# Kernel optimization log

Measured on AMD Instinct MI355X. Metric: run time of the kernel, lower is better.

## Reference

```python
import jax, jax.numpy as jnp
import numpy as np

N = 20000          # nodes
E = 320000         # edges
H = 128            # hidden_channels
A = 512            # aerial feature dim
SPOT = 20000
DIST_UNIT = 50
NEMB = SPOT // DIST_UNIT
RATIO = 0.25       # neighbor_ratio


def setup_inputs() -> dict:
    key = jax.random.key(0)
    ks = jax.random.split(key, 12)
    x = jax.random.normal(ks[0], (N, H), jnp.float32)
    edge_index = jax.random.randint(ks[1], (2, E), 0, N)
    distances = jax.random.randint(ks[2], (E,), 0, SPOT)
    aerial_emb = jax.random.normal(ks[3], (N, A), jnp.float32)
    s = lambda k, shape, fan: jax.random.normal(k, shape, jnp.float32) / np.sqrt(fan).astype(np.float32)
    W_lin = s(ks[4], (H, H), H)
    b_lin = jnp.zeros((H,), jnp.float32)
    W_q = s(ks[5], (H + A + H, H), H + A + H)
    b_q = jnp.zeros((H,), jnp.float32)
    W_v = s(ks[6], (H, H), H)
    b_v = jnp.zeros((H,), jnp.float32)
    dist_table = jax.random.normal(ks[7], (NEMB, H), jnp.float32)  # init.normal_ like torch
    W_l = s(ks[8], (H, H), H)   # SAGE lin_l (neighbor aggr), with bias
    b_l = jnp.zeros((H,), jnp.float32)
    W_r = s(ks[9], (H, H), H)   # SAGE lin_r (root), no bias in PyG default
    return dict(x=x, edge_index=edge_index, distances=distances, aerial_emb=aerial_emb,
                W_lin=W_lin, b_lin=b_lin, W_q=W_q, b_q=b_q, W_v=W_v, b_v=b_v,
                dist_table=dist_table, W_l=W_l, b_l=b_l, W_r=W_r)


def reference(x, edge_index, distances, aerial_emb, W_lin, b_lin, W_q, b_q, W_v, b_v, dist_table, W_l, b_l, W_r):
    n = x.shape[0]
    e = edge_index.shape[1]
    k = int(e * RATIO)  # static: number of sampled edges

    x = x @ W_lin + b_lin                                  # [N, H]
    src, tgt = edge_index[0], edge_index[1]
    source_x = x[src]                                      # [E, H]
    target_x = x[tgt]                                      # [E, H]
    source_aerial = aerial_emb[src]                        # [E, A]
    dist_x = dist_table[distances // DIST_UNIT]            # [E, H]

    query = jnp.concatenate([source_x, source_aerial, dist_x], axis=1) @ W_q + b_q  # [E, H]
    value = target_x @ W_v + b_v                           # [E, H]
    logits = -jnp.linalg.norm(query - value, axis=1)       # [E]
    logprob = jax.nn.log_softmax(logits, axis=0)

    # torch.multinomial(prob, k) without replacement == Gumbel top-k on log-probs
    u = jax.random.uniform(jax.random.key(42), (e,), jnp.float32)
    gumbel = -jnp.log(-jnp.log(u + 1e-20) + 1e-20)
    _, sel = jax.lax.top_k(logprob + gumbel, k)            # [k] selected edge ids
    src_s = src[sel]
    tgt_s = tgt[sel]

    # SAGEConv (mean aggregation): out = lin_l(mean_j x_j) + lin_r(x)
    msg = jax.ops.segment_sum(x[src_s], tgt_s, num_segments=n)              # [N, H]
    deg = jax.ops.segment_sum(jnp.ones((k,), x.dtype), tgt_s, num_segments=n)
    aggr = msg / jnp.maximum(deg, 1.0)[:, None]
    out = aggr @ W_l + b_l + x @ W_r                       # [N, H]
    return out
```

## Files before the change

kernel.cpp:

```cpp
#include <hip/hip_runtime.h>
#include <stdint.h>

#define N_NODES 20000
#define E_EDGES 320000
#define H_DIM 128
#define A_DIM 512
#define NEMB_N 400
#define K_SEL 80000u
#define NB1 16384
#define NB2 16384
#define CAND_MAX 8192
#define LO_F (-128.0f)
#define SCALE1 (16384.0f / 160.0f)

struct SelState {
    int b1; unsigned cum1; unsigned r1;
    int b2; unsigned cum2; unsigned r2;
    unsigned long long T;
};

__device__ __forceinline__ uint32_t rotl32(uint32_t x, int r) {
    return (x << r) | (x >> (32 - r));
}

__device__ __forceinline__ void threefry2x32(uint32_t k0, uint32_t k1,
                                             uint32_t& x0, uint32_t& x1) {
    uint32_t ks0 = k0, ks1 = k1, ks2 = k0 ^ k1 ^ 0x1BD11BDAu;
    x0 += ks0; x1 += ks1;
    x0 += x1; x1 = rotl32(x1, 13); x1 ^= x0;
    x0 += x1; x1 = rotl32(x1, 15); x1 ^= x0;
    x0 += x1; x1 = rotl32(x1, 26); x1 ^= x0;
    x0 += x1; x1 = rotl32(x1, 6);  x1 ^= x0;
    x0 += ks1; x1 += ks2 + 1u;
    x0 += x1; x1 = rotl32(x1, 17); x1 ^= x0;
    x0 += x1; x1 = rotl32(x1, 29); x1 ^= x0;
    x0 += x1; x1 = rotl32(x1, 16); x1 ^= x0;
    x0 += x1; x1 = rotl32(x1, 24); x1 ^= x0;
    x0 += ks2; x1 += ks0 + 2u;
    x0 += x1; x1 = rotl32(x1, 13); x1 ^= x0;
    x0 += x1; x1 = rotl32(x1, 15); x1 ^= x0;
    x0 += x1; x1 = rotl32(x1, 26); x1 ^= x0;
    x0 += x1; x1 = rotl32(x1, 6);  x1 ^= x0;
    x0 += ks0; x1 += ks1 + 3u;
    x0 += x1; x1 = rotl32(x1, 17); x1 ^= x0;
    x0 += x1; x1 = rotl32(x1, 29); x1 ^= x0;
    x0 += x1; x1 = rotl32(x1, 16); x1 ^= x0;
    x0 += x1; x1 = rotl32(x1, 24); x1 ^= x0;
    x0 += ks1; x1 += ks2 + 4u;
    x0 += x1; x1 = rotl32(x1, 13); x1 ^= x0;
    x0 += x1; x1 = rotl32(x1, 15); x1 ^= x0;
    x0 += x1; x1 = rotl32(x1, 26); x1 ^= x0;
    x0 += x1; x1 = rotl32(x1, 6);  x1 ^= x0;
    x0 += ks2; x1 += ks0 + 5u;
}

__global__ __launch_bounds__(256) void k_rand(float* __restrict__ u) {
    int e = blockIdx.x * 256 + threadIdx.x;
    if (e >= E_EDGES) return;
    uint32_t x0 = 0u, x1 = (uint32_t)e;
    threefry2x32(0u, 42u, x0, x1);
    uint32_t bits = x0 ^ x1;
    uint32_t fb = (bits >> 9) | 0x3f800000u;
    u[e] = __uint_as_float(fb) - 1.0f;
}

__global__ __launch_bounds__(128) void k_node(
    const float* __restrict__ x, const float* __restrict__ aerial,
    const float* __restrict__ Wlin, const float* __restrict__ blin,
    const float* __restrict__ Wq, const float* __restrict__ bq,
    const float* __restrict__ Wv, const float* __restrict__ bv,
    float* __restrict__ xl32, float* __restrict__ q32, float* __restrict__ v32) {
    __shared__ float xinT[H_DIM][8];
    __shared__ float xsT[H_DIM][8];
    __shared__ float aerT[A_DIM][8];
    const int j = threadIdx.x;
    const int n0 = blockIdx.x * 8;
#pragma unroll
    for (int m = 0; m < 8; ++m) xinT[j][m] = x[(size_t)(n0 + m) * H_DIM + j];
#pragma unroll
    for (int m = 0; m < 8; ++m)
#pragma unroll
        for (int c = 0; c < 4; ++c)
            aerT[c * H_DIM + j][m] = aerial[(size_t)(n0 + m) * A_DIM + c * H_DIM + j];
    __syncthreads();
    float acc[8];
    {
        float bj = blin[j];
#pragma unroll
        for (int m = 0; m < 8; ++m) acc[m] = bj;
        for (int k = 0; k < H_DIM; ++k) {
            float w = Wlin[k * H_DIM + j];
            const float4* xp = (const float4*)&xinT[k][0];
            float4 a0 = xp[0], a1 = xp[1];
            acc[0] = fmaf(a0.x, w, acc[0]); acc[1] = fmaf(a0.y, w, acc[1]);
            acc[2] = fmaf(a0.z, w, acc[2]); acc[3] = fmaf(a0.w, w, acc[3]);
            acc[4] = fmaf(a1.x, w, acc[4]); acc[5] = fmaf(a1.y, w, acc[5]);
            acc[6] = fmaf(a1.z, w, acc[6]); acc[7] = fmaf(a1.w, w, acc[7]);
        }
    }
#pragma unroll
    for (int m = 0; m < 8; ++m) {
        xsT[j][m] = acc[m];
        xl32[(size_t)(n0 + m) * H_DIM + j] = acc[m];
    }
    __syncthreads();
    {
        float bj = bv[j];
        float av[8];
#pragma unroll
        for (int m = 0; m < 8; ++m) av[m] = bj;
        for (int k = 0; k < H_DIM; ++k) {
            float w = Wv[k * H_DIM + j];
            const float4* xp = (const float4*)&xsT[k][0];
            float4 a0 = xp[0], a1 = xp[1];
            av[0] = fmaf(a0.x, w, av[0]); av[1] = fmaf(a0.y, w, av[1]);
            av[2] = fmaf(a0.z, w, av[2]); av[3] = fmaf(a0.w, w, av[3]);
            av[4] = fmaf(a1.x, w, av[4]); av[5] = fmaf(a1.y, w, av[5]);
            av[6] = fmaf(a1.z, w, av[6]); av[7] = fmaf(a1.w, w, av[7]);
        }
#pragma unroll
        for (int m = 0; m < 8; ++m) v32[(size_t)(n0 + m) * H_DIM + j] = av[m];
    }
    {
        float bj = bq[j];
        float aq[8];
#pragma unroll
        for (int m = 0; m < 8; ++m) aq[m] = bj;
        for (int k = 0; k < H_DIM; ++k) {
            float w = Wq[k * H_DIM + j];
            const float4* xp = (const float4*)&xsT[k][0];
            float4 a0 = xp[0], a1 = xp[1];
            aq[0] = fmaf(a0.x, w, aq[0]); aq[1] = fmaf(a0.y, w, aq[1]);
            aq[2] = fmaf(a0.z, w, aq[2]); aq[3] = fmaf(a0.w, w, aq[3]);
            aq[4] = fmaf(a1.x, w, aq[4]); aq[5] = fmaf(a1.y, w, aq[5]);
            aq[6] = fmaf(a1.z, w, aq[6]); aq[7] = fmaf(a1.w, w, aq[7]);
        }
        for (int k = 0; k < A_DIM; ++k) {
            float w = Wq[(size_t)(H_DIM + k) * H_DIM + j];
            const float4* xp = (const float4*)&aerT[k][0];
            float4 a0 = xp[0], a1 = xp[1];
            aq[0] = fmaf(a0.x, w, aq[0]); aq[1] = fmaf(a0.y, w, aq[1]);
            aq[2] = fmaf(a0.z, w, aq[2]); aq[3] = fmaf(a0.w, w, aq[3]);
            aq[4] = fmaf(a1.x, w, aq[4]); aq[5] = fmaf(a1.y, w, aq[5]);
            aq[6] = fmaf(a1.z, w, aq[6]); aq[7] = fmaf(a1.w, w, aq[7]);
        }
#pragma unroll
        for (int m = 0; m < 8; ++m) q32[(size_t)(n0 + m) * H_DIM + j] = aq[m];
    }
}

__global__ __launch_bounds__(128) void k_dist(
    const float* __restrict__ dtab, const float* __restrict__ Wq,
    float* __restrict__ dq32) {
    __shared__ float dsT[H_DIM][8];
    const int j = threadIdx.x;
    const int n0 = blockIdx.x * 8;
#pragma unroll
    for (int m = 0; m < 8; ++m) dsT[j][m] = dtab[(size_t)(n0 + m) * H_DIM + j];
    __syncthreads();
    float acc[8];
#pragma unroll
    for (int m = 0; m < 8; ++m) acc[m] = 0.0f;
    for (int k = 0; k < H_DIM; ++k) {
        float w = Wq[(size_t)(H_DIM + A_DIM + k) * H_DIM + j];
        const float4* xp = (const float4*)&dsT[k][0];
        float4 a0 = xp[0], a1 = xp[1];
        acc[0] = fmaf(a0.x, w, acc[0]); acc[1] = fmaf(a0.y, w, acc[1]);
        acc[2] = fmaf(a0.z, w, acc[2]); acc[3] = fmaf(a0.w, w, acc[3]);
        acc[4] = fmaf(a1.x, w, acc[4]); acc[5] = fmaf(a1.y, w, acc[5]);
        acc[6] = fmaf(a1.z, w, acc[6]); acc[7] = fmaf(a1.w, w, acc[7]);
    }
#pragma unroll
    for (int m = 0; m < 8; ++m) dq32[(size_t)(n0 + m) * H_DIM + j] = acc[m];
}

__device__ __forceinline__ int bin1_of(float s) {
    float t = (s - LO_F) * SCALE1;
    int b = (int)t;
    return min(max(b, 0), NB1 - 1);
}
__device__ __forceinline__ int bin2_of(float s, int b1) {
    float t = (s - LO_F) * SCALE1;
    float frac = t - (float)b1;
    int b = (int)(frac * (float)NB2);
    return min(max(b, 0), NB2 - 1);
}

__global__ __launch_bounds__(256) void k_score(
    const int* __restrict__ ei, const int* __restrict__ dist,
    const float* __restrict__ q32, const float* __restrict__ v32,
    const float* __restrict__ dq32, const float* __restrict__ u,
    unsigned long long* __restrict__ keys, float* __restrict__ s32o,
    unsigned* __restrict__ hist1) {
    const int half = threadIdx.x >> 5, lane = threadIdx.x & 31;
    const int e = blockIdx.x * 8 + half;
    const int s = ei[e], t = ei[E_EDGES + e];
    const int db = dist[e] / 50;
    const float4* qp = (const float4*)(q32 + (size_t)s * H_DIM);
    const float4* vp = (const float4*)(v32 + (size_t)t * H_DIM);
    const float4* dp = (const float4*)(dq32 + (size_t)db * H_DIM);
    float4 q = qp[lane], v = vp[lane], d = dp[lane];
    float dx = q.x + d.x - v.x;
    float dy = q.y + d.y - v.y;
    float dz = q.z + d.z - v.z;
    float dw = q.w + d.w - v.w;
    float ss = fmaf(dx, dx, fmaf(dy, dy, fmaf(dz, dz, dw * dw)));
#pragma unroll
    for (int o = 16; o > 0; o >>= 1) ss += __shfl_xor(ss, o, 64);
    if (lane == 0) {
        float nrm = sqrtf(ss);
        float uu = u[e];
        float a = -logf(uu + 1e-20f);
        float g = -logf(a + 1e-20f);
        float score = g - nrm;
        int ib = __float_as_int(score);
        unsigned m32 = (ib < 0) ? ~(unsigned)ib : ((unsigned)ib | 0x80000000u);
        keys[e] = ((unsigned long long)m32 << 32) | (unsigned)(0xFFFFFFFFu - (unsigned)e);
        s32o[e] = score;
        atomicAdd(&hist1[bin1_of(score)], 1u);
    }
}

__global__ __launch_bounds__(256) void k_hist2(const float* __restrict__ s32,
                                               const SelState* __restrict__ st,
                                               unsigned* __restrict__ hist2) {
    int e = blockIdx.x * 256 + threadIdx.x;
    if (e >= E_EDGES) return;
    float s = s32[e];
    int b1 = bin1_of(s);
    if (b1 != st->b1) return;
    atomicAdd(&hist2[bin2_of(s, b1)], 1u);
}

__global__ __launch_bounds__(256) void k_scan(const unsigned* __restrict__ hist,
                                              SelState* st, int phase) {
    __shared__ unsigned csum[256];
    __shared__ unsigned bins[64];
    __shared__ int selc;
    __shared__ unsigned cumbase;
    const int t = threadIdx.x;
    const unsigned target = (phase == 1) ? K_SEL : st->r1;
    unsigned s = 0;
    for (int i = 0; i < 64; ++i) s += hist[t * 64 + i];
    csum[t] = s;
    __syncthreads();
    if (t == 0) {
        unsigned cum = 0; int c = 255;
        for (; c >= 0; --c) {
            if (cum + csum[c] >= target) break;
            cum += csum[c];
        }
        selc = c; cumbase = cum;
    }
    __syncthreads();
    if (t < 64) bins[t] = hist[selc * 64 + t];
    __syncthreads();
    if (t == 0) {
        unsigned cum = cumbase; int b = -1;
        for (int i = 63; i >= 0; --i) {
            if (cum + bins[i] >= target) { b = selc * 64 + i; break; }
            cum += bins[i];
        }
        unsigned r = target - cum;
        if (phase == 1) { st->b1 = b; st->cum1 = cum; st->r1 = r; }
        else           { st->b2 = b; st->cum2 = cum; st->r2 = r; }
    }
}

__global__ __launch_bounds__(256) void k_collect(
    const float* __restrict__ s32, const unsigned long long* __restrict__ keys,
    const SelState* __restrict__ st, unsigned long long* __restrict__ cand,
    unsigned* __restrict__ cnt) {
    int e = blockIdx.x * 256 + threadIdx.x;
    if (e >= E_EDGES) return;
    float s = s32[e];
    int b1 = bin1_of(s);
    if (b1 != st->b1) return;
    if (bin2_of(s, b1) != st->b2) return;
    unsigned p = atomicAdd(cnt, 1u);
    if (p < CAND_MAX) cand[p] = keys[e];
}

__global__ __launch_bounds__(256) void k_thresh(
    const unsigned long long* __restrict__ cand, const unsigned* __restrict__ cnt,
    SelState* st) {
    int c = (int)min(*cnt, (unsigned)CAND_MAX);
    unsigned r2 = st->r2;
    for (int i = threadIdx.x; i < c; i += blockDim.x) {
        unsigned long long ki = cand[i];
        unsigned g = 0;
        for (int j = 0; j < c; ++j) g += (cand[j] > ki);
        if (g == r2 - 1) st->T = ki;
    }
}

__global__ __launch_bounds__(256) void k_scatter(
    const int* __restrict__ ei, const unsigned long long* __restrict__ keys,
    const SelState* __restrict__ st, const float* __restrict__ xl32,
    float* __restrict__ msg, float* __restrict__ deg) {
    const int wid = threadIdx.x >> 6, lane = threadIdx.x & 63;
    const int e = blockIdx.x * 4 + wid;
    if (keys[e] >= st->T) {
        int sidx = ei[e], tidx = ei[E_EDGES + e];
        const float* xp = xl32 + (size_t)sidx * H_DIM;
        float* mp = msg + (size_t)tidx * H_DIM;
        const int h = lane * 2;
        atomicAdd(&mp[h], xp[h]);
        atomicAdd(&mp[h + 1], xp[h + 1]);
        if (lane == 0) atomicAdd(&deg[tidx], 1.0f);
    }
}

__global__ __launch_bounds__(128) void k_out(
    const float* __restrict__ msg, const float* __restrict__ deg,
    const float* __restrict__ xl32, const float* __restrict__ Wl,
    const float* __restrict__ bl, const float* __restrict__ Wr,
    float* __restrict__ out) {
    __shared__ float axT[H_DIM][8];
    __shared__ float xxT[H_DIM][8];
    const int j = threadIdx.x;
    const int n0 = blockIdx.x * 8;
#pragma unroll
    for (int m = 0; m < 8; ++m) {
        float d = fmaxf(deg[n0 + m], 1.0f);
        axT[j][m] = msg[(size_t)(n0 + m) * H_DIM + j] / d;
        xxT[j][m] = xl32[(size_t)(n0 + m) * H_DIM + j];
    }
    __syncthreads();
    float acc[8];
    float bj = bl[j];
#pragma unroll
    for (int m = 0; m < 8; ++m) acc[m] = bj;
    for (int k = 0; k < H_DIM; ++k) {
        float wl = Wl[k * H_DIM + j];
        float wr = Wr[k * H_DIM + j];
        const float4* ap = (const float4*)&axT[k][0];
        const float4* xp = (const float4*)&xxT[k][0];
        float4 a0 = ap[0], a1 = ap[1];
        float4 x0 = xp[0], x1 = xp[1];
        acc[0] = fmaf(a0.x, wl, fmaf(x0.x, wr, acc[0]));
        acc[1] = fmaf(a0.y, wl, fmaf(x0.y, wr, acc[1]));
        acc[2] = fmaf(a0.z, wl, fmaf(x0.z, wr, acc[2]));
        acc[3] = fmaf(a0.w, wl, fmaf(x0.w, wr, acc[3]));
        acc[4] = fmaf(a1.x, wl, fmaf(x1.x, wr, acc[4]));
        acc[5] = fmaf(a1.y, wl, fmaf(x1.y, wr, acc[5]));
        acc[6] = fmaf(a1.z, wl, fmaf(x1.z, wr, acc[6]));
        acc[7] = fmaf(a1.w, wl, fmaf(x1.w, wr, acc[7]));
    }
#pragma unroll
    for (int m = 0; m < 8; ++m) out[(size_t)(n0 + m) * H_DIM + j] = acc[m];
}

extern "C" void kernel_launch(void* const* d_in, const int* in_sizes, int n_in,
                              void* d_out, int out_size, void* d_ws, size_t ws_size,
                              hipStream_t stream) {
    const float* x      = (const float*)d_in[0];
    const int*   ei     = (const int*)d_in[1];
    const int*   dist   = (const int*)d_in[2];
    const float* aerial = (const float*)d_in[3];
    const float* Wlin   = (const float*)d_in[4];
    const float* blin   = (const float*)d_in[5];
    const float* Wq     = (const float*)d_in[6];
    const float* bq     = (const float*)d_in[7];
    const float* Wv     = (const float*)d_in[8];
    const float* bv     = (const float*)d_in[9];
    const float* dtab   = (const float*)d_in[10];
    const float* Wl     = (const float*)d_in[11];
    const float* bl     = (const float*)d_in[12];
    const float* Wr     = (const float*)d_in[13];
    float* out = (float*)d_out;

    char* ws = (char*)d_ws;
    size_t off = 0;
    auto alloc = [&](size_t bytes) -> void* {
        void* p = ws + off;
        off += (bytes + 255) & ~(size_t)255;
        return p;
    };
    float* q32  = (float*)alloc((size_t)N_NODES * H_DIM * 4);
    float* v32  = (float*)alloc((size_t)N_NODES * H_DIM * 4);
    float* dq32 = (float*)alloc((size_t)NEMB_N * H_DIM * 4);
    unsigned long long* keys = (unsigned long long*)alloc((size_t)E_EDGES * 8);
    float* xl32 = (float*)alloc((size_t)N_NODES * H_DIM * 4);
    float* urnd = (float*)alloc((size_t)E_EDGES * 4);
    float* s32  = (float*)alloc((size_t)E_EDGES * 4);
    char* zbase = ws + off;
    float* msg  = (float*)alloc((size_t)N_NODES * H_DIM * 4);
    float* deg  = (float*)alloc((size_t)N_NODES * 4);
    unsigned* hist1 = (unsigned*)alloc((size_t)NB1 * 4);
    unsigned* hist2 = (unsigned*)alloc((size_t)NB2 * 4);
    unsigned long long* cand = (unsigned long long*)alloc((size_t)CAND_MAX * 8);
    unsigned* counters = (unsigned*)alloc(256);
    SelState* st = (SelState*)alloc(256);
    size_t zlen = (size_t)((ws + off) - zbase);

    hipMemsetAsync(zbase, 0, zlen, stream);

    k_node<<<N_NODES / 8, 128, 0, stream>>>(x, aerial, Wlin, blin, Wq, bq, Wv, bv,
                                            xl32, q32, v32);
    k_dist<<<NEMB_N / 8, 128, 0, stream>>>(dtab, Wq, dq32);
    k_rand<<<(E_EDGES + 255) / 256, 256, 0, stream>>>(urnd);
    k_score<<<E_EDGES / 8, 256, 0, stream>>>(ei, dist, q32, v32, dq32, urnd, keys, s32, hist1);
    k_scan<<<1, 256, 0, stream>>>(hist1, st, 1);
    k_hist2<<<(E_EDGES + 255) / 256, 256, 0, stream>>>(s32, st, hist2);
    k_scan<<<1, 256, 0, stream>>>(hist2, st, 2);
    k_collect<<<(E_EDGES + 255) / 256, 256, 0, stream>>>(s32, keys, st, cand, &counters[0]);
    k_thresh<<<1, 256, 0, stream>>>(cand, &counters[0], st);
    k_scatter<<<E_EDGES / 4, 256, 0, stream>>>(ei, keys, st, xl32, msg, deg);
    k_out<<<N_NODES / 8, 128, 0, stream>>>(msg, deg, xl32, Wl, bl, Wr, out);
}
```

Measured before the change: 553.9 us.

## Counting-sort edges by source node and swizzle block order for gather locality

Adds a counting sort of the edges by source node (histogram, single-block prefix scan, atomic placement), so the score and scatter kernels walk edges grouped by source and reuse the q32/xl32 rows they gather. Block indices in those kernels are swizzled across the 8 groups, presumably to spread work over the XCDs. Keys and scores are stored in sorted order while keeping the original edge id in the key, so selection results and tie-breaking stay the same. The cost is three extra kernel launches, extra atomics and about 16 bytes per edge of extra index traffic, which are meant to be repaid by better cache hits on the gathers.

```diff
diff --git a/kernel.cpp b/kernel.cpp
--- a/kernel.cpp
+++ b/kernel.cpp
@@ -174,6 +174,51 @@
     for (int m = 0; m < 8; ++m) dq32[(size_t)(n0 + m) * H_DIM + j] = acc[m];
 }
 
+__global__ __launch_bounds__(256) void k_hist_src(const int* __restrict__ ei,
+                                                  unsigned* __restrict__ cnt) {
+    int e = blockIdx.x * 256 + threadIdx.x;
+    if (e >= E_EDGES) return;
+    atomicAdd(&cnt[ei[e]], 1u);
+}
+
+__global__ __launch_bounds__(256) void k_prefix(const unsigned* __restrict__ cnt,
+                                                unsigned* __restrict__ off) {
+    __shared__ unsigned ssum[256];
+    const int t = threadIdx.x;
+    const int PER = (N_NODES + 255) / 256;
+    unsigned s = 0;
+    for (int i = 0; i < PER; ++i) {
+        int idx = t * PER + i;
+        if (idx < N_NODES) s += cnt[idx];
+    }
+    ssum[t] = s;
+    __syncthreads();
+    if (t == 0) {
+        unsigned acc = 0;
+        for (int i = 0; i < 256; ++i) { unsigned v = ssum[i]; ssum[i] = acc; acc += v; }
+    }
+    __syncthreads();
+    unsigned run = ssum[t];
+    for (int i = 0; i < PER; ++i) {
+        int idx = t * PER + i;
+        if (idx < N_NODES) { off[idx] = run; run += cnt[idx]; }
+    }
+}
+
+__global__ __launch_bounds__(256) void k_place(
+    const int* __restrict__ ei, const int* __restrict__ dist,
+    unsigned* __restrict__ off_work, int* __restrict__ srcsort,
+    int* __restrict__ tgtsort, int* __restrict__ dbsort, int* __restrict__ esort) {
+    int e = blockIdx.x * 256 + threadIdx.x;
+    if (e >= E_EDGES) return;
+    int s = ei[e];
+    unsigned pos = atomicAdd(&off_work[s], 1u);
+    srcsort[pos] = s;
+    tgtsort[pos] = ei[E_EDGES + e];
+    dbsort[pos] = dist[e] / 50;
+    esort[pos] = e;
+}
+
 __device__ __forceinline__ int bin1_of(float s) {
     float t = (s - LO_F) * SCALE1;
     int b = (int)t;
@@ -187,15 +232,19 @@
 }
 
 __global__ __launch_bounds__(256) void k_score(
-    const int* __restrict__ ei, const int* __restrict__ dist,
+    const int* __restrict__ srcsort, const int* __restrict__ tgtsort,
+    const int* __restrict__ dbsort, const int* __restrict__ esort,
     const float* __restrict__ q32, const float* __restrict__ v32,
     const float* __restrict__ dq32, const float* __restrict__ u,
-    unsigned long long* __restrict__ keys, float* __restrict__ s32o,
+    unsigned long long* __restrict__ keys_s, float* __restrict__ s32o,
     unsigned* __restrict__ hist1) {
     const int half = threadIdx.x >> 5, lane = threadIdx.x & 31;
-    const int e = blockIdx.x * 8 + half;
-    const int s = ei[e], t = ei[E_EDGES + e];
-    const int db = dist[e] / 50;
+    const int nb = E_EDGES / 8;
+    const int bid = blockIdx.x;
+    const int swz = (bid & 7) * (nb >> 3) + (bid >> 3);
+    const int i = swz * 8 + half;
+    const int s = srcsort[i], t = tgtsort[i];
+    const int db = dbsort[i];
     const float4* qp = (const float4*)(q32 + (size_t)s * H_DIM);
     const float4* vp = (const float4*)(v32 + (size_t)t * H_DIM);
     const float4* dp = (const float4*)(dq32 + (size_t)db * H_DIM);
@@ -208,6 +257,7 @@
 #pragma unroll
     for (int o = 16; o > 0; o >>= 1) ss += __shfl_xor(ss, o, 64);
     if (lane == 0) {
+        const int e = esort[i];
         float nrm = sqrtf(ss);
         float uu = u[e];
         float a = -logf(uu + 1e-20f);
@@ -215,8 +265,8 @@
         float score = g - nrm;
         int ib = __float_as_int(score);
         unsigned m32 = (ib < 0) ? ~(unsigned)ib : ((unsigned)ib | 0x80000000u);
-        keys[e] = ((unsigned long long)m32 << 32) | (unsigned)(0xFFFFFFFFu - (unsigned)e);
-        s32o[e] = score;
+        keys_s[i] = ((unsigned long long)m32 << 32) | (unsigned)(0xFFFFFFFFu - (unsigned)e);
+        s32o[i] = score;
         atomicAdd(&hist1[bin1_of(score)], 1u);
     }
 }
@@ -295,13 +345,17 @@
 }
 
 __global__ __launch_bounds__(256) void k_scatter(
-    const int* __restrict__ ei, const unsigned long long* __restrict__ keys,
+    const int* __restrict__ srcsort, const int* __restrict__ tgtsort,
+    const unsigned long long* __restrict__ keys_s,
     const SelState* __restrict__ st, const float* __restrict__ xl32,
     float* __restrict__ msg, float* __restrict__ deg) {
     const int wid = threadIdx.x >> 6, lane = threadIdx.x & 63;
-    const int e = blockIdx.x * 4 + wid;
-    if (keys[e] >= st->T) {
-        int sidx = ei[e], tidx = ei[E_EDGES + e];
+    const int nb = E_EDGES / 4;
+    const int bid = blockIdx.x;
+    const int swz = (bid & 7) * (nb >> 3) + (bid >> 3);
+    const int i = swz * 4 + wid;
+    if (keys_s[i] >= st->T) {
+        int sidx = srcsort[i], tidx = tgtsort[i];
         const float* xp = xl32 + (size_t)sidx * H_DIM;
         float* mp = msg + (size_t)tidx * H_DIM;
         const int h = lane * 2;
@@ -380,15 +434,21 @@
     float* q32  = (float*)alloc((size_t)N_NODES * H_DIM * 4);
     float* v32  = (float*)alloc((size_t)N_NODES * H_DIM * 4);
     float* dq32 = (float*)alloc((size_t)NEMB_N * H_DIM * 4);
-    unsigned long long* keys = (unsigned long long*)alloc((size_t)E_EDGES * 8);
     float* xl32 = (float*)alloc((size_t)N_NODES * H_DIM * 4);
     float* urnd = (float*)alloc((size_t)E_EDGES * 4);
-    float* s32  = (float*)alloc((size_t)E_EDGES * 4);
+    int* srcsort = (int*)alloc((size_t)E_EDGES * 4);
+    int* tgtsort = (int*)alloc((size_t)E_EDGES * 4);
+    int* dbsort  = (int*)alloc((size_t)E_EDGES * 4);
+    int* esort   = (int*)alloc((size_t)E_EDGES * 4);
+    unsigned long long* keys_s = (unsigned long long*)alloc((size_t)E_EDGES * 8);
+    float* s32_s = (float*)alloc((size_t)E_EDGES * 4);
+    unsigned* off_work = (unsigned*)alloc((size_t)N_NODES * 4);
     char* zbase = ws + off;
     float* msg  = (float*)alloc((size_t)N_NODES * H_DIM * 4);
     float* deg  = (float*)alloc((size_t)N_NODES * 4);
     unsigned* hist1 = (unsigned*)alloc((size_t)NB1 * 4);
     unsigned* hist2 = (unsigned*)alloc((size_t)NB2 * 4);
+    unsigned* cnt_src = (unsigned*)alloc((size_t)N_NODES * 4);
     unsigned long long* cand = (unsigned long long*)alloc((size_t)CAND_MAX * 8);
     unsigned* counters = (unsigned*)alloc(256);
     SelState* st = (SelState*)alloc(256);
@@ -396,16 +456,23 @@
 
     hipMemsetAsync(zbase, 0, zlen, stream);
 
+    k_hist_src<<<(E_EDGES + 255) / 256, 256, 0, stream>>>(ei, cnt_src);
+    k_prefix<<<1, 256, 0, stream>>>(cnt_src, off_work);
+    k_place<<<(E_EDGES + 255) / 256, 256, 0, stream>>>(ei, dist, off_work,
+                                                       srcsort, tgtsort, dbsort, esort);
+
     k_node<<<N_NODES / 8, 128, 0, stream>>>(x, aerial, Wlin, blin, Wq, bq, Wv, bv,
                                             xl32, q32, v32);
     k_dist<<<NEMB_N / 8, 128, 0, stream>>>(dtab, Wq, dq32);
     k_rand<<<(E_EDGES + 255) / 256, 256, 0, stream>>>(urnd);
-    k_score<<<E_EDGES / 8, 256, 0, stream>>>(ei, dist, q32, v32, dq32, urnd, keys, s32, hist1);
+
+    k_score<<<E_EDGES / 8, 256, 0, stream>>>(srcsort, tgtsort, dbsort, esort,
+                                             q32, v32, dq32, urnd, keys_s, s32_s, hist1);
     k_scan<<<1, 256, 0, stream>>>(hist1, st, 1);
-    k_hist2<<<(E_EDGES + 255) / 256, 256, 0, stream>>>(s32, st, hist2);
+    k_hist2<<<(E_EDGES + 255) / 256, 256, 0, stream>>>(s32_s, st, hist2);
     k_scan<<<1, 256, 0, stream>>>(hist2, st, 2);
-    k_collect<<<(E_EDGES + 255) / 256, 256, 0, stream>>>(s32, keys, st, cand, &counters[0]);
+    k_collect<<<(E_EDGES + 255) / 256, 256, 0, stream>>>(s32_s, keys_s, st, cand, &counters[0]);
     k_thresh<<<1, 256, 0, stream>>>(cand, &counters[0], st);
-    k_scatter<<<E_EDGES / 4, 256, 0, stream>>>(ei, keys, st, xl32, msg, deg);
+    k_scatter<<<E_EDGES / 4, 256, 0, stream>>>(srcsort, tgtsort, keys_s, st, xl32, msg, deg);
     k_out<<<N_NODES / 8, 128, 0, stream>>>(msg, deg, xl32, Wl, bl, Wr, out);
 }
```

Result: slower. 641.0 us (+15.7%).
